# Performance work log

Measured on AMD Instinct MI355X. Metric: run time of the kernel, lower is better.

## Reference

```python
import jax, jax.numpy as jnp
import numpy as np

B, C, S, D = 16, 32, 64, 512
DFF, E = 2048, 8


def setup_inputs() -> dict:
    key = jax.random.key(0)
    ks = jax.random.split(key, 16)
    std = 0.02
    return {
        'x': jax.random.normal(ks[0], (B, C, S, D), jnp.float32),
        'baseline': jax.random.normal(ks[1], (B, C, S, D), jnp.float32),
        'attnres': jax.random.normal(ks[2], (B, C, S, D), jnp.float32),
        'shared_w1': jax.random.normal(ks[3], (DFF, D), jnp.float32) * std,
        'shared_b1': jnp.zeros((DFF,), jnp.float32),
        'shared_w2': jax.random.normal(ks[4], (D, DFF), jnp.float32) * std,
        'shared_b2': jnp.zeros((D,), jnp.float32),
        'spa_router_w': jax.random.normal(ks[5], (E, 3 * D), jnp.float32) * std,
        'spa_router_b': jnp.zeros((E,), jnp.float32),
        'spe_router_w': jax.random.normal(ks[6], (E, 3 * D), jnp.float32) * std,
        'spe_router_b': jnp.zeros((E,), jnp.float32),
        'spa_w1': jax.random.normal(ks[7], (E, DFF, D), jnp.float32) * std,
        'spa_b1': jnp.zeros((E, DFF), jnp.float32),
        'spa_w2': jax.random.normal(ks[8], (E, D, DFF), jnp.float32) * std,
        'spa_b2': jnp.zeros((E, D), jnp.float32),
        'spe_w1': jax.random.normal(ks[9], (E, DFF, D), jnp.float32) * std,
        'spe_b1': jnp.zeros((E, DFF), jnp.float32),
        'spe_w2': jax.random.normal(ks[10], (E, D, DFF), jnp.float32) * std,
        'spe_b2': jnp.zeros((E, D), jnp.float32),
    }


def _route(feat, rw, rb):
    # feat [B, 3D] -> top-1 expert index [B] and its softmax gate weight [B]
    logits = feat @ rw.T + rb            # [B, E]
    p = jax.nn.softmax(logits, axis=-1)
    idx = jnp.argmax(logits, axis=-1)    # [B]
    w = jnp.take_along_axis(p, idx[:, None], axis=-1)[:, 0]
    return idx, w


def _specialist(xf, idx, w1, b1, w2, b2):
    # xf [B, T, D]; per-sample gather of expert weights then batched FFN
    W1, B1 = w1[idx], b1[idx]            # [B, DFF, D], [B, DFF]
    W2, B2 = w2[idx], b2[idx]            # [B, D, DFF], [B, D]
    h = jax.nn.gelu(jnp.einsum('btd,bfd->btf', xf, W1) + B1[:, None, :])
    return jnp.einsum('btf,bdf->btd', h, W2) + B2[:, None, :]


def reference(x, baseline, attnres, shared_w1, shared_b1, shared_w2, shared_b2,
              spa_router_w, spa_router_b, spe_router_w, spe_router_b,
              spa_w1, spa_b1, spa_w2, spa_b2, spe_w1, spe_b1, spe_w2, spe_b2):
    b, d = x.shape[0], x.shape[-1]
    xf = x.reshape(b, -1, d)  # [B, T, D]
    # sample-level AttnRes router features: [B, 3*d_model]
    feat = jnp.concatenate([
        baseline.mean(axis=(1, 2)),
        attnres.mean(axis=(1, 2)),
        (attnres - baseline).mean(axis=(1, 2)),
    ], axis=-1)
    spa_idx, spa_w = _route(feat, spa_router_w, spa_router_b)
    spe_idx, spe_w = _route(feat, spe_router_w, spe_router_b)
    # shared dense FFN (dropout=0 eval)
    shared = jax.nn.gelu(xf @ shared_w1.T + shared_b1) @ shared_w2.T + shared_b2
    spa_out = _specialist(xf, spa_idx, spa_w1, spa_b1, spa_w2, spa_b2)
    spe_out = _specialist(xf, spe_idx, spe_w1, spe_b1, spe_w2, spe_b2)
    y = shared + spa_w[:, None, None] * spa_out + spe_w[:, None, None] * spe_out
    return y.reshape(x.shape)
```

## Files before the change

kernel.cpp:

```cpp
#include <hip/hip_runtime.h>
#include <cstdint>
#include <cstddef>

#define DEV __device__ __forceinline__

typedef unsigned short u16;
typedef _Float16 f16x8 __attribute__((ext_vector_type(8)));
typedef float f32x4 __attribute__((ext_vector_type(4)));

static constexpr int NB  = 16;
static constexpr int T   = 2048;
static constexpr int D   = 512;
static constexpr int DFF = 2048;
static constexpr int NE  = 8;
static constexpr int FEAT = 3 * D;

#define MFMA16 __builtin_amdgcn_mfma_f32_16x16x32_f16

DEV u16 f2h(float f) {
  _Float16 h = (_Float16)f;
  union { _Float16 h; u16 u; } cv; cv.h = h; return cv.u;
}

DEV float gelu_fast(float x) {
  const float t = x * x;
  const float p = x * fmaf(t, -0.07135481627f, -1.59576912161f);
  return __fdividef(x, 1.0f + __expf(p));
}


__global__ void k_part(const float* __restrict__ base, const float* __restrict__ attn,
                       float* __restrict__ part) {
  const int b = blockIdx.x >> 4, ch = blockIdx.x & 15;
  const int d = threadIdx.x;
  const size_t o = ((size_t)b * T + (size_t)ch * 128) * D + d;
  const float* pb = base + o;
  const float* pa = attn + o;
  float sb = 0.f, sa = 0.f;
  for (int r = 0; r < 128; ++r) { sb += pb[(size_t)r * D]; sa += pa[(size_t)r * D]; }
  part[(b * 16 + ch) * D + d] = sb;
  part[NB * 16 * D + (b * 16 + ch) * D + d] = sa;
}

__global__ void k_feat(const float* __restrict__ part, float* __restrict__ feat) {
  const int b = blockIdx.x, d = threadIdx.x;
  float sb = 0.f, sa = 0.f;
  for (int ch = 0; ch < 16; ++ch) {
    sb += part[(b * 16 + ch) * D + d];
    sa += part[NB * 16 * D + (b * 16 + ch) * D + d];
  }
  sb *= (1.0f / 2048.0f); sa *= (1.0f / 2048.0f);
  feat[b * FEAT + d] = sb;
  feat[b * FEAT + D + d] = sa;
  feat[b * FEAT + 2 * D + d] = sa - sb;
}

__global__ void k_route(const float* __restrict__ feat,
                        const float* __restrict__ rw0, const float* __restrict__ rb0,
                        const float* __restrict__ rw1, const float* __restrict__ rb1,
                        int* __restrict__ idx, float* __restrict__ gate) {
  const int r = blockIdx.x >> 4, b = blockIdx.x & 15;
  const float* rw = (r == 0) ? rw0 : rw1;
  const float* rb = (r == 0) ? rb0 : rb1;
  const int l = threadIdx.x;
  float p[8];
#pragma unroll
  for (int e = 0; e < 8; ++e) p[e] = 0.f;
  const float* f = feat + b * FEAT;
  for (int k = l; k < FEAT; k += 64) {
    const float fv = f[k];
#pragma unroll
    for (int e = 0; e < 8; ++e) p[e] += fv * rw[e * FEAT + k];
  }
#pragma unroll
  for (int off = 32; off >= 1; off >>= 1) {
#pragma unroll
    for (int e = 0; e < 8; ++e) p[e] += __shfl_xor(p[e], off);
  }
  if (l == 0) {
    float best = -1e30f; int bi = 0;
    float lg[8];
#pragma unroll
    for (int e = 0; e < 8; ++e) {
      lg[e] = p[e] + rb[e];
      if (lg[e] > best) { best = lg[e]; bi = e; }
    }
    float s = 0.f;
#pragma unroll
    for (int e = 0; e < 8; ++e) s += expf(lg[e] - best);
    idx[r * 16 + b] = bi;
    gate[r * 16 + b] = 1.0f / s;
  }
}

__global__ void k_btot(const float* __restrict__ b2s, const float* __restrict__ b2a,
                       const float* __restrict__ b2e, const int* __restrict__ idx,
                       const float* __restrict__ gate, float* __restrict__ btot) {
  const int b = blockIdx.x, d = threadIdx.x;
  const int ia = idx[b], ie = idx[16 + b];
  const float ga = gate[b], ge = gate[16 + b];
  btot[b * D + d] = b2s[d] + ga * b2a[ia * D + d] + ge * b2e[ie * D + d];
}

__global__ void k_cast(const float* __restrict__ s, u16* __restrict__ d, long n) {
  const long i = ((long)blockIdx.x * blockDim.x + threadIdx.x) * 4;
  if (i >= n) return;
  const float4 v = *(const float4*)(s + i);
  const unsigned int lo = (unsigned int)f2h(v.x) | ((unsigned int)f2h(v.y) << 16);
  const unsigned int hi = (unsigned int)f2h(v.z) | ((unsigned int)f2h(v.w) << 16);
  *(uint2*)(d + i) = make_uint2(lo, hi);
}


DEV void ld_lds16(const void* g, void* l) {
  __builtin_amdgcn_global_load_lds((const __attribute__((address_space(1))) void*)g,
                                   (__attribute__((address_space(3))) void*)l, 16, 0, 0);
}

template <int NC>
DEV void gemm_pipe(const u16* __restrict__ A, int lda, const u16* __restrict__ B, int ldb,
                   u16* As, u16* Bs, f32x4 (&acc)[8][4]) {
  static_assert(NC >= 4, "pipeline needs >=4 chunks");
  const int tid = threadIdx.x;
  const int lane = tid & 63, wid = tid >> 6;
  const int wr = wid >> 2, wc = wid & 3;

  const int r0 = wid * 32 + (lane >> 2);
  const int r1 = r0 + 16;
  const int cb0 = (lane & 3) ^ ((r0 >> 1) & 3);
  const int cb1 = (lane & 3) ^ ((r1 >> 1) & 3);
  const int ldsO0 = wid * 1024;
  const int ldsO1 = wid * 1024 + 512;
  const u16* gA0 = A + (size_t)r0 * lda + cb0 * 8;
  const u16* gA1 = A + (size_t)r1 * lda + cb1 * 8;
  const u16* gB0 = B + (size_t)r0 * ldb + cb0 * 8;
  const u16* gB1 = B + (size_t)r1 * ldb + cb1 * 8;

  const int kb = lane >> 4;
  int ar[8], br[4];
#pragma unroll
  for (int m = 0; m < 8; ++m) {
    const int R = wr * 128 + m * 16 + (lane & 15);
    ar[m] = R * 64 + ((kb ^ ((R >> 1) & 3)) * 16);
  }
#pragma unroll
  for (int n = 0; n < 4; ++n) {
    const int C = wc * 64 + n * 16 + (lane & 15);
    br[n] = C * 64 + ((kb ^ ((C >> 1) & 3)) * 16);
  }

  {
    const u16 *a0 = gA0, *a1 = gA1, *b0 = gB0, *b1 = gB1;
#pragma unroll
    for (int c = 0; c < 3; ++c) {
      ld_lds16(a0, As + c * 8192 + ldsO0);
      ld_lds16(a1, As + c * 8192 + ldsO1);
      ld_lds16(b0, Bs + c * 8192 + ldsO0);
      ld_lds16(b1, Bs + c * 8192 + ldsO1);
      a0 += 32; a1 += 32; b0 += 32; b1 += 32;
    }
  }
  const u16 *sA0 = gA0 + 96, *sA1 = gA1 + 96, *sB0 = gB0 + 96, *sB1 = gB1 + 96;
  asm volatile("s_waitcnt vmcnt(8)" ::: "memory");
  __builtin_amdgcn_s_barrier();

  for (int ch = 0; ch < NC; ++ch) {
    const char* Asl = (const char*)(As + (ch & 3) * 8192);
    const char* Bsl = (const char*)(Bs + (ch & 3) * 8192);
    const bool st = (ch + 3) < NC;
    const int ssl = (ch + 3) & 3;

    f16x8 av[8], bv0, bv1, bv2, bv3;
#pragma unroll
    for (int m = 0; m < 8; ++m) av[m] = *(const f16x8*)(Asl + ar[m]);
    bv0 = *(const f16x8*)(Bsl + br[0]);
    bv1 = *(const f16x8*)(Bsl + br[1]);
    if (st) {
      ld_lds16(sA0, As + ssl * 8192 + ldsO0);
      ld_lds16(sA1, As + ssl * 8192 + ldsO1);
    }
    __builtin_amdgcn_s_barrier();
    asm volatile("s_waitcnt lgkmcnt(0)" ::: "memory");
    __builtin_amdgcn_s_setprio(1);
#pragma unroll
    for (int m = 0; m < 8; ++m) {
      acc[m][0] = MFMA16(av[m], bv0, acc[m][0], 0, 0, 0);
      acc[m][1] = MFMA16(av[m], bv1, acc[m][1], 0, 0, 0);
    }
    __builtin_amdgcn_s_setprio(0);
    __builtin_amdgcn_s_barrier();

    bv2 = *(const f16x8*)(Bsl + br[2]);
    bv3 = *(const f16x8*)(Bsl + br[3]);
    if (st) {
      ld_lds16(sB0, Bs + ssl * 8192 + ldsO0);
      ld_lds16(sB1, Bs + ssl * 8192 + ldsO1);
    }
    __builtin_amdgcn_s_barrier();
    asm volatile("s_waitcnt lgkmcnt(0)" ::: "memory");
    __builtin_amdgcn_s_setprio(1);
#pragma unroll
    for (int m = 0; m < 8; ++m) {
      acc[m][2] = MFMA16(av[m], bv2, acc[m][2], 0, 0, 0);
      acc[m][3] = MFMA16(av[m], bv3, acc[m][3], 0, 0, 0);
    }
    __builtin_amdgcn_s_setprio(0);
    sA0 += 32; sA1 += 32; sB0 += 32; sB1 += 32;

    if (ch < NC - 3)       asm volatile("s_waitcnt vmcnt(8)" ::: "memory");
    else if (ch == NC - 3) asm volatile("s_waitcnt vmcnt(4)" ::: "memory");
    else if (ch == NC - 2) asm volatile("s_waitcnt vmcnt(0)" ::: "memory");
    __builtin_amdgcn_s_barrier();
  }
}

template <int BANK>
__global__ __launch_bounds__(512, 2) void k_ffn1(
    const u16* __restrict__ xh, const u16* __restrict__ w1, const float* __restrict__ b1,
    const int* __restrict__ idx, const float* __restrict__ gate, u16* __restrict__ h) {
  __shared__ alignas(16) u16 As[4 * 8192];
  __shared__ alignas(16) u16 Bs[4 * 8192];
  int wg = blockIdx.x;
  const int q = (int)gridDim.x >> 3;
  wg = (wg & 7) * q + (wg >> 3);
  const int b  = wg >> 6;
  const int mt = (wg >> 3) & 7;
  const int nt = wg & 7;

  const int e   = (BANK == 0) ? 0 : idx[(BANK - 1) * 16 + b];
  const float g = (BANK == 0) ? 1.0f : gate[(BANK - 1) * 16 + b];
  const u16* Ab = xh + ((size_t)b * T + (size_t)mt * 256) * D;
  const u16* Bb = w1 + (size_t)e * DFF * D + (size_t)nt * 256 * D;
  const float* bb = b1 + (size_t)e * DFF;

  f32x4 acc[8][4];
#pragma unroll
  for (int m = 0; m < 8; ++m)
#pragma unroll
    for (int n = 0; n < 4; ++n)
#pragma unroll
      for (int r = 0; r < 4; ++r) acc[m][n][r] = 0.f;

  gemm_pipe<16>(Ab, D, Bb, D, As, Bs, acc);

  const int lane = threadIdx.x & 63, wid = threadIdx.x >> 6;
  const int wr = wid >> 2, wc = wid & 3;
  const int rr = (lane >> 4) << 2, cc = lane & 15;
  const int mrow = mt * 256 + wr * 128;
  const int ncol = nt * 256 + wc * 64;
  u16* hb = h + (size_t)b * T * DFF;
  float bias[4];
#pragma unroll
  for (int n = 0; n < 4; ++n) bias[n] = bb[ncol + n * 16 + cc];
#pragma unroll
  for (int m = 0; m < 8; ++m) {
    const int row = mrow + m * 16 + rr;
#pragma unroll
    for (int n = 0; n < 4; ++n) {
      const int col = ncol + n * 16 + cc;
      const f32x4 a = acc[m][n];
#pragma unroll
      for (int r = 0; r < 4; ++r) {
        const float v = gelu_fast(a[r] + bias[n]) * g;
        hb[(size_t)(row + r) * DFF + col] = f2h(v);
      }
    }
  }
}

template <int BANK>
__global__ __launch_bounds__(512, 2) void k_ffn2(
    const u16* __restrict__ h, const u16* __restrict__ w2, const float* __restrict__ btot,
    const int* __restrict__ idx, float* __restrict__ out) {
  __shared__ alignas(16) u16 As[4 * 8192];
  __shared__ alignas(16) u16 Bs[4 * 8192];
  int wg = blockIdx.x;
  const int q = (int)gridDim.x >> 3;
  wg = (wg & 7) * q + (wg >> 3);
  const int b  = wg >> 4;
  const int mt = (wg >> 1) & 7;
  const int nt = wg & 1;

  const int e = (BANK == 0) ? 0 : idx[(BANK - 1) * 16 + b];
  const u16* Ab = h + ((size_t)b * T + (size_t)mt * 256) * DFF;
  const u16* Bb = w2 + (size_t)e * D * DFF + (size_t)nt * 256 * DFF;

  f32x4 acc[8][4];
#pragma unroll
  for (int m = 0; m < 8; ++m)
#pragma unroll
    for (int n = 0; n < 4; ++n)
#pragma unroll
      for (int r = 0; r < 4; ++r) acc[m][n][r] = 0.f;

  gemm_pipe<64>(Ab, DFF, Bb, DFF, As, Bs, acc);

  const int lane = threadIdx.x & 63, wid = threadIdx.x >> 6;
  const int wr = wid >> 2, wc = wid & 3;
  const int rr = (lane >> 4) << 2, cc = lane & 15;
  const int mrow = mt * 256 + wr * 128;
  const int ncol = nt * 256 + wc * 64;
  float* ob = out + (size_t)b * T * D;
  float bt[4];
#pragma unroll
  for (int n = 0; n < 4; ++n) bt[n] = btot[b * D + ncol + n * 16 + cc];
#pragma unroll
  for (int m = 0; m < 8; ++m) {
    const int row = mrow + m * 16 + rr;
#pragma unroll
    for (int n = 0; n < 4; ++n) {
      const int col = ncol + n * 16 + cc;
      const f32x4 a = acc[m][n];
#pragma unroll
      for (int r = 0; r < 4; ++r) {
        const size_t oi = (size_t)(row + r) * D + col;
        if (BANK == 0) ob[oi] = a[r] + bt[n];
        else           ob[oi] += a[r];
      }
    }
  }
}


extern "C" void kernel_launch(void* const* d_in, const int* in_sizes, int n_in,
                              void* d_out, int out_size, void* d_ws, size_t ws_size,
                              hipStream_t stream) {
  (void)in_sizes; (void)n_in; (void)out_size; (void)ws_size;
  const float* x    = (const float*)d_in[0];
  const float* base = (const float*)d_in[1];
  const float* attn = (const float*)d_in[2];
  const float* sw1  = (const float*)d_in[3];
  const float* sb1  = (const float*)d_in[4];
  const float* sw2  = (const float*)d_in[5];
  const float* sb2  = (const float*)d_in[6];
  const float* arw  = (const float*)d_in[7];
  const float* arb  = (const float*)d_in[8];
  const float* erw  = (const float*)d_in[9];
  const float* erb  = (const float*)d_in[10];
  const float* aw1  = (const float*)d_in[11];
  const float* ab1  = (const float*)d_in[12];
  const float* aw2  = (const float*)d_in[13];
  const float* ab2  = (const float*)d_in[14];
  const float* ew1  = (const float*)d_in[15];
  const float* eb1  = (const float*)d_in[16];
  const float* ew2  = (const float*)d_in[17];
  const float* eb2  = (const float*)d_in[18];
  float* out = (float*)d_out;

  char* w = (char*)d_ws;
  u16* xh   = (u16*)w;  w += (size_t)NB * T * D * 2;
  u16* hbuf = (u16*)w;  w += (size_t)NB * T * DFF * 2;
  u16* w1s  = (u16*)w;  w += (size_t)DFF * D * 2;
  u16* w2s  = (u16*)w;  w += (size_t)D * DFF * 2;
  u16* w1a  = (u16*)w;  w += (size_t)NE * DFF * D * 2;
  u16* w2a  = (u16*)w;  w += (size_t)NE * D * DFF * 2;
  u16* w1e  = (u16*)w;  w += (size_t)NE * DFF * D * 2;
  u16* w2e  = (u16*)w;  w += (size_t)NE * D * DFF * 2;
  float* part = (float*)w; w += (size_t)2 * NB * 16 * D * 4;
  float* feat = (float*)w; w += (size_t)NB * FEAT * 4;
  int*   idx  = (int*)w;   w += 32 * 4;
  float* gate = (float*)w; w += 32 * 4;
  float* btot = (float*)w; w += (size_t)NB * D * 4;

  k_part<<<dim3(256), dim3(512), 0, stream>>>(base, attn, part);
  k_feat<<<dim3(16), dim3(512), 0, stream>>>(part, feat);
  k_route<<<dim3(32), dim3(64), 0, stream>>>(feat, arw, arb, erw, erb, idx, gate);
  k_btot<<<dim3(16), dim3(512), 0, stream>>>(sb2, ab2, eb2, idx, gate, btot);

  {
    long n;
    n = (long)NB * T * D;      k_cast<<<(unsigned)(n / 1024), 256, 0, stream>>>(x,   xh,  n);
    n = (long)DFF * D;         k_cast<<<(unsigned)(n / 1024), 256, 0, stream>>>(sw1, w1s, n);
    n = (long)D * DFF;         k_cast<<<(unsigned)(n / 1024), 256, 0, stream>>>(sw2, w2s, n);
    n = (long)NE * DFF * D;    k_cast<<<(unsigned)(n / 1024), 256, 0, stream>>>(aw1, w1a, n);
    n = (long)NE * D * DFF;    k_cast<<<(unsigned)(n / 1024), 256, 0, stream>>>(aw2, w2a, n);
    n = (long)NE * DFF * D;    k_cast<<<(unsigned)(n / 1024), 256, 0, stream>>>(ew1, w1e, n);
    n = (long)NE * D * DFF;    k_cast<<<(unsigned)(n / 1024), 256, 0, stream>>>(ew2, w2e, n);
  }

  const dim3 g1(1024), g2(256), blk(512);
  k_ffn1<0><<<g1, blk, 0, stream>>>(xh, w1s, sb1, idx, gate, hbuf);
  k_ffn2<0><<<g2, blk, 0, stream>>>(hbuf, w2s, btot, idx, out);
  k_ffn1<1><<<g1, blk, 0, stream>>>(xh, w1a, ab1, idx, gate, hbuf);
  k_ffn2<1><<<g2, blk, 0, stream>>>(hbuf, w2a, btot, idx, out);
  k_ffn1<2><<<g1, blk, 0, stream>>>(xh, w1e, eb1, idx, gate, hbuf);
  k_ffn2<2><<<g2, blk, 0, stream>>>(hbuf, w2e, btot, idx, out);
}
```

Measured before the change: 737.1 us.

## Double-buffer GEMM pipeline, raise occupancy, narrow FFN2 tiles, skip unused expert casts

The GEMM pipeline drops from four LDS stages to two, which halves shared memory per block so launch bounds can allow four blocks per CU. FFN2 gets a narrower N tile (128 instead of 256), doubling its grid to fill the GPU better. The router now marks which experts are selected, and the weight casts skip experts nobody uses, cutting conversion traffic. The cost is a shallower prefetch, so global-load latency is hidden less, and FFN2 makes more redundant A-tile reads.

```diff
diff --git a/kernel.cpp b/kernel.cpp
--- a/kernel.cpp
+++ b/kernel.cpp
@@ -55,10 +55,15 @@
   feat[b * FEAT + 2 * D + d] = sa - sb;
 }
 
+__global__ void k_zero(int* __restrict__ used) {
+  used[threadIdx.x] = 0;
+}
+
 __global__ void k_route(const float* __restrict__ feat,
                         const float* __restrict__ rw0, const float* __restrict__ rb0,
                         const float* __restrict__ rw1, const float* __restrict__ rb1,
-                        int* __restrict__ idx, float* __restrict__ gate) {
+                        int* __restrict__ idx, float* __restrict__ gate,
+                        int* __restrict__ used) {
   const int r = blockIdx.x >> 4, b = blockIdx.x & 15;
   const float* rw = (r == 0) ? rw0 : rw1;
   const float* rb = (r == 0) ? rb0 : rb1;
@@ -90,6 +95,7 @@
     for (int e = 0; e < 8; ++e) s += expf(lg[e] - best);
     idx[r * 16 + b] = bi;
     gate[r * 16 + b] = 1.0f / s;
+    atomicOr(&used[r * 8 + bi], 1);
   }
 }
 
@@ -111,6 +117,17 @@
   *(uint2*)(d + i) = make_uint2(lo, hi);
 }
 
+__global__ void k_cast_gated(const float* __restrict__ s, u16* __restrict__ d,
+                             const int* __restrict__ used) {
+  const int e = blockIdx.x >> 10;
+  if (!used[e]) return;
+  const long i = (long)e * (DFF * D) + ((long)(blockIdx.x & 1023) * 256 + threadIdx.x) * 4;
+  const float4 v = *(const float4*)(s + i);
+  const unsigned int lo = (unsigned int)f2h(v.x) | ((unsigned int)f2h(v.y) << 16);
+  const unsigned int hi = (unsigned int)f2h(v.z) | ((unsigned int)f2h(v.w) << 16);
+  *(uint2*)(d + i) = make_uint2(lo, hi);
+}
+
 
 DEV void ld_lds16(const void* g, void* l) {
   __builtin_amdgcn_global_load_lds((const __attribute__((address_space(1))) void*)g,
@@ -118,9 +135,8 @@
 }
 
 template <int NC>
-DEV void gemm_pipe(const u16* __restrict__ A, int lda, const u16* __restrict__ B, int ldb,
-                   u16* As, u16* Bs, f32x4 (&acc)[8][4]) {
-  static_assert(NC >= 4, "pipeline needs >=4 chunks");
+DEV void gemm_pipe1(const u16* __restrict__ A, int lda, const u16* __restrict__ B, int ldb,
+                    u16* As, u16* Bs, f32x4 (&acc)[8][4]) {
   const int tid = threadIdx.x;
   const int lane = tid & 63, wid = tid >> 6;
   const int wr = wid >> 2, wc = wid & 3;
@@ -149,26 +165,19 @@
     br[n] = C * 64 + ((kb ^ ((C >> 1) & 3)) * 16);
   }
 
-  {
-    const u16 *a0 = gA0, *a1 = gA1, *b0 = gB0, *b1 = gB1;
-#pragma unroll
-    for (int c = 0; c < 3; ++c) {
-      ld_lds16(a0, As + c * 8192 + ldsO0);
-      ld_lds16(a1, As + c * 8192 + ldsO1);
-      ld_lds16(b0, Bs + c * 8192 + ldsO0);
-      ld_lds16(b1, Bs + c * 8192 + ldsO1);
-      a0 += 32; a1 += 32; b0 += 32; b1 += 32;
-    }
-  }
-  const u16 *sA0 = gA0 + 96, *sA1 = gA1 + 96, *sB0 = gB0 + 96, *sB1 = gB1 + 96;
-  asm volatile("s_waitcnt vmcnt(8)" ::: "memory");
+  ld_lds16(gA0, As + ldsO0);
+  ld_lds16(gA1, As + ldsO1);
+  ld_lds16(gB0, Bs + ldsO0);
+  ld_lds16(gB1, Bs + ldsO1);
+  const u16 *sA0 = gA0 + 32, *sA1 = gA1 + 32, *sB0 = gB0 + 32, *sB1 = gB1 + 32;
+  asm volatile("s_waitcnt vmcnt(0)" ::: "memory");
   __builtin_amdgcn_s_barrier();
 
   for (int ch = 0; ch < NC; ++ch) {
-    const char* Asl = (const char*)(As + (ch & 3) * 8192);
-    const char* Bsl = (const char*)(Bs + (ch & 3) * 8192);
-    const bool st = (ch + 3) < NC;
-    const int ssl = (ch + 3) & 3;
+    const char* Asl = (const char*)(As + (ch & 1) * 8192);
+    const char* Bsl = (const char*)(Bs + (ch & 1) * 8192);
+    const bool st = (ch + 1) < NC;
+    const int ssl = (ch + 1) & 1;
 
     f16x8 av[8], bv0, bv1, bv2, bv3;
 #pragma unroll
@@ -196,7 +205,6 @@
       ld_lds16(sB0, Bs + ssl * 8192 + ldsO0);
       ld_lds16(sB1, Bs + ssl * 8192 + ldsO1);
     }
-    __builtin_amdgcn_s_barrier();
     asm volatile("s_waitcnt lgkmcnt(0)" ::: "memory");
     __builtin_amdgcn_s_setprio(1);
 #pragma unroll
@@ -206,20 +214,87 @@
     }
     __builtin_amdgcn_s_setprio(0);
     sA0 += 32; sA1 += 32; sB0 += 32; sB1 += 32;
-
-    if (ch < NC - 3)       asm volatile("s_waitcnt vmcnt(8)" ::: "memory");
-    else if (ch == NC - 3) asm volatile("s_waitcnt vmcnt(4)" ::: "memory");
-    else if (ch == NC - 2) asm volatile("s_waitcnt vmcnt(0)" ::: "memory");
+    if (st) asm volatile("s_waitcnt vmcnt(0)" ::: "memory");
     __builtin_amdgcn_s_barrier();
   }
 }
 
+template <int NC>
+DEV void gemm_pipe2(const u16* __restrict__ A, int lda, const u16* __restrict__ B, int ldb,
+                    u16* As, u16* Bs, f32x4 (&acc)[8][2]) {
+  const int tid = threadIdx.x;
+  const int lane = tid & 63, wid = tid >> 6;
+  const int wr = wid >> 2, wc = wid & 3;
+
+  const int r0 = wid * 32 + (lane >> 2);
+  const int r1 = r0 + 16;
+  const int rb_ = wid * 16 + (lane >> 2);
+  const int cb0 = (lane & 3) ^ ((r0 >> 1) & 3);
+  const int cb1 = (lane & 3) ^ ((r1 >> 1) & 3);
+  const int cbB = (lane & 3) ^ ((rb_ >> 1) & 3);
+  const int ldsO0 = wid * 1024;
+  const int ldsO1 = wid * 1024 + 512;
+  const int ldsOB = wid * 512;
+  const u16* gA0 = A + (size_t)r0 * lda + cb0 * 8;
+  const u16* gA1 = A + (size_t)r1 * lda + cb1 * 8;
+  const u16* gB0 = B + (size_t)rb_ * ldb + cbB * 8;
+
+  const int kb = lane >> 4;
+  int ar[8], br[2];
+#pragma unroll
+  for (int m = 0; m < 8; ++m) {
+    const int R = wr * 128 + m * 16 + (lane & 15);
+    ar[m] = R * 64 + ((kb ^ ((R >> 1) & 3)) * 16);
+  }
+#pragma unroll
+  for (int n = 0; n < 2; ++n) {
+    const int C = wc * 32 + n * 16 + (lane & 15);
+    br[n] = C * 64 + ((kb ^ ((C >> 1) & 3)) * 16);
+  }
+
+  ld_lds16(gA0, As + ldsO0);
+  ld_lds16(gA1, As + ldsO1);
+  ld_lds16(gB0, Bs + ldsOB);
+  const u16 *sA0 = gA0 + 32, *sA1 = gA1 + 32, *sB0 = gB0 + 32;
+  asm volatile("s_waitcnt vmcnt(0)" ::: "memory");
+  __builtin_amdgcn_s_barrier();
+
+  for (int ch = 0; ch < NC; ++ch) {
+    const char* Asl = (const char*)(As + (ch & 1) * 8192);
+    const char* Bsl = (const char*)(Bs + (ch & 1) * 4096);
+    const bool st = (ch + 1) < NC;
+    const int ssl = (ch + 1) & 1;
+
+    f16x8 av[8], bv0, bv1;
+#pragma unroll
+    for (int m = 0; m < 8; ++m) av[m] = *(const f16x8*)(Asl + ar[m]);
+    bv0 = *(const f16x8*)(Bsl + br[0]);
+    bv1 = *(const f16x8*)(Bsl + br[1]);
+    if (st) {
+      ld_lds16(sA0, As + ssl * 8192 + ldsO0);
+      ld_lds16(sA1, As + ssl * 8192 + ldsO1);
+      ld_lds16(sB0, Bs + ssl * 4096 + ldsOB);
+      sA0 += 32; sA1 += 32; sB0 += 32;
+    }
+    asm volatile("s_waitcnt lgkmcnt(0)" ::: "memory");
+    __builtin_amdgcn_s_setprio(1);
+#pragma unroll
+    for (int m = 0; m < 8; ++m) {
+      acc[m][0] = MFMA16(av[m], bv0, acc[m][0], 0, 0, 0);
+      acc[m][1] = MFMA16(av[m], bv1, acc[m][1], 0, 0, 0);
+    }
+    __builtin_amdgcn_s_setprio(0);
+    if (st) asm volatile("s_waitcnt vmcnt(0)" ::: "memory");
+    __builtin_amdgcn_s_barrier();
+  }
+}
+
 template <int BANK>
-__global__ __launch_bounds__(512, 2) void k_ffn1(
+__global__ __launch_bounds__(512, 4) void k_ffn1(
     const u16* __restrict__ xh, const u16* __restrict__ w1, const float* __restrict__ b1,
     const int* __restrict__ idx, const float* __restrict__ gate, u16* __restrict__ h) {
-  __shared__ alignas(16) u16 As[4 * 8192];
-  __shared__ alignas(16) u16 Bs[4 * 8192];
+  __shared__ alignas(16) u16 As[2 * 8192];
+  __shared__ alignas(16) u16 Bs[2 * 8192];
   int wg = blockIdx.x;
   const int q = (int)gridDim.x >> 3;
   wg = (wg & 7) * q + (wg >> 3);
@@ -241,7 +316,7 @@
 #pragma unroll
       for (int r = 0; r < 4; ++r) acc[m][n][r] = 0.f;
 
-  gemm_pipe<16>(Ab, D, Bb, D, As, Bs, acc);
+  gemm_pipe1<16>(Ab, D, Bb, D, As, Bs, acc);
 
   const int lane = threadIdx.x & 63, wid = threadIdx.x >> 6;
   const int wr = wid >> 2, wc = wid & 3;
@@ -269,46 +344,46 @@
 }
 
 template <int BANK>
-__global__ __launch_bounds__(512, 2) void k_ffn2(
+__global__ __launch_bounds__(512, 4) void k_ffn2(
     const u16* __restrict__ h, const u16* __restrict__ w2, const float* __restrict__ btot,
     const int* __restrict__ idx, float* __restrict__ out) {
-  __shared__ alignas(16) u16 As[4 * 8192];
-  __shared__ alignas(16) u16 Bs[4 * 8192];
+  __shared__ alignas(16) u16 As[2 * 8192];
+  __shared__ alignas(16) u16 Bs[2 * 4096];
   int wg = blockIdx.x;
   const int q = (int)gridDim.x >> 3;
   wg = (wg & 7) * q + (wg >> 3);
-  const int b  = wg >> 4;
-  const int mt = (wg >> 1) & 7;
-  const int nt = wg & 1;
+  const int b  = wg >> 5;
+  const int mt = (wg >> 2) & 7;
+  const int nt = wg & 3;
 
   const int e = (BANK == 0) ? 0 : idx[(BANK - 1) * 16 + b];
   const u16* Ab = h + ((size_t)b * T + (size_t)mt * 256) * DFF;
-  const u16* Bb = w2 + (size_t)e * D * DFF + (size_t)nt * 256 * DFF;
-
-  f32x4 acc[8][4];
+  const u16* Bb = w2 + (size_t)e * D * DFF + (size_t)nt * 128 * DFF;
+
+  f32x4 acc[8][2];
 #pragma unroll
   for (int m = 0; m < 8; ++m)
 #pragma unroll
-    for (int n = 0; n < 4; ++n)
+    for (int n = 0; n < 2; ++n)
 #pragma unroll
       for (int r = 0; r < 4; ++r) acc[m][n][r] = 0.f;
 
-  gemm_pipe<64>(Ab, DFF, Bb, DFF, As, Bs, acc);
+  gemm_pipe2<64>(Ab, DFF, Bb, DFF, As, Bs, acc);
 
   const int lane = threadIdx.x & 63, wid = threadIdx.x >> 6;
   const int wr = wid >> 2, wc = wid & 3;
   const int rr = (lane >> 4) << 2, cc = lane & 15;
   const int mrow = mt * 256 + wr * 128;
-  const int ncol = nt * 256 + wc * 64;
+  const int ncol = nt * 128 + wc * 32;
   float* ob = out + (size_t)b * T * D;
-  float bt[4];
-#pragma unroll
-  for (int n = 0; n < 4; ++n) bt[n] = btot[b * D + ncol + n * 16 + cc];
+  float bt[2];
+#pragma unroll
+  for (int n = 0; n < 2; ++n) bt[n] = btot[b * D + ncol + n * 16 + cc];
 #pragma unroll
   for (int m = 0; m < 8; ++m) {
     const int row = mrow + m * 16 + rr;
 #pragma unroll
-    for (int n = 0; n < 4; ++n) {
+    for (int n = 0; n < 2; ++n) {
       const int col = ncol + n * 16 + cc;
       const f32x4 a = acc[m][n];
 #pragma unroll
@@ -361,24 +436,26 @@
   int*   idx  = (int*)w;   w += 32 * 4;
   float* gate = (float*)w; w += 32 * 4;
   float* btot = (float*)w; w += (size_t)NB * D * 4;
-
+  int*   used = (int*)w;   w += 16 * 4;
+
+  k_zero<<<dim3(1), dim3(16), 0, stream>>>(used);
   k_part<<<dim3(256), dim3(512), 0, stream>>>(base, attn, part);
   k_feat<<<dim3(16), dim3(512), 0, stream>>>(part, feat);
-  k_route<<<dim3(32), dim3(64), 0, stream>>>(feat, arw, arb, erw, erb, idx, gate);
+  k_route<<<dim3(32), dim3(64), 0, stream>>>(feat, arw, arb, erw, erb, idx, gate, used);
   k_btot<<<dim3(16), dim3(512), 0, stream>>>(sb2, ab2, eb2, idx, gate, btot);
 
   {
     long n;
-    n = (long)NB * T * D;      k_cast<<<(unsigned)(n / 1024), 256, 0, stream>>>(x,   xh,  n);
-    n = (long)DFF * D;         k_cast<<<(unsigned)(n / 1024), 256, 0, stream>>>(sw1, w1s, n);
-    n = (long)D * DFF;         k_cast<<<(unsigned)(n / 1024), 256, 0, stream>>>(sw2, w2s, n);
-    n = (long)NE * DFF * D;    k_cast<<<(unsigned)(n / 1024), 256, 0, stream>>>(aw1, w1a, n);
-    n = (long)NE * D * DFF;    k_cast<<<(unsigned)(n / 1024), 256, 0, stream>>>(aw2, w2a, n);
-    n = (long)NE * DFF * D;    k_cast<<<(unsigned)(n / 1024), 256, 0, stream>>>(ew1, w1e, n);
-    n = (long)NE * D * DFF;    k_cast<<<(unsigned)(n / 1024), 256, 0, stream>>>(ew2, w2e, n);
-  }
-
-  const dim3 g1(1024), g2(256), blk(512);
+    n = (long)NB * T * D;  k_cast<<<(unsigned)(n / 1024), 256, 0, stream>>>(x,   xh,  n);
+    n = (long)DFF * D;     k_cast<<<(unsigned)(n / 1024), 256, 0, stream>>>(sw1, w1s, n);
+    n = (long)D * DFF;     k_cast<<<(unsigned)(n / 1024), 256, 0, stream>>>(sw2, w2s, n);
+    k_cast_gated<<<dim3(8192), 256, 0, stream>>>(aw1, w1a, used);
+    k_cast_gated<<<dim3(8192), 256, 0, stream>>>(aw2, w2a, used);
+    k_cast_gated<<<dim3(8192), 256, 0, stream>>>(ew1, w1e, used + 8);
+    k_cast_gated<<<dim3(8192), 256, 0, stream>>>(ew2, w2e, used + 8);
+  }
+
+  const dim3 g1(1024), g2(512), blk(512);
   k_ffn1<0><<<g1, blk, 0, stream>>>(xh, w1s, sb1, idx, gate, hbuf);
   k_ffn2<0><<<g2, blk, 0, stream>>>(hbuf, w2s, btot, idx, out);
   k_ffn1<1><<<g1, blk, 0, stream>>>(xh, w1a, ab1, idx, gate, hbuf);
```

Measured after the change: 2.215 ms. 201% more time.
